# Kernel tuning notes

Measured on AMD Instinct MI355X. Metric: run time of the kernel, lower is better.

The kernel has to match this reference:

```python
import jax, jax.numpy as jnp
import numpy as np

NUM_JOINT_LIST = [8, 10, 12, 14, 16, 18, 20, 22, 24, 9, 13, 17]
NUM_GLOBAL_LIST = [1, 0, 1, 1, 0, 1, 1, 1, 0, 1, 1, 1]
M = len(NUM_JOINT_LIST)
B, T, JMAX = 16, 128, 24
H, HEADS, L, RANK = 256, 8, 4, 8
DH = H // HEADS
LAYERSCALE = 1e-4


def setup_inputs():
    key = jax.random.key(0)
    ks = jax.random.split(key, 40)
    m_idx = jax.random.randint(ks[0], (B,), 0, M)
    nj = jnp.array(NUM_JOINT_LIST)[m_idx]
    valid = jnp.arange(JMAX)[None, :] < nj[:, None]  # (B, J) real joints of each morphology
    jtype = jax.random.randint(ks[1], (B, JMAX), 0, 3)  # 0 slide, 1 hinge, 2 global
    has_g = (jnp.array(NUM_GLOBAL_LIST) > 0)[m_idx][:, None]
    jtype = jnp.where((jtype == 2) & ~has_g, 0, jtype)
    tile = lambda m: jnp.broadcast_to(m[:, None, :], (B, T, JMAX))
    slide_mask = tile((jtype == 0) & valid)
    hinge_mask = tile((jtype == 1) & valid)
    global_mask = tile((jtype == 2) & valid)
    act_mask = tile(valid)
    morph_mask = (valid[:, :, None] & valid[:, None, :]) | jnp.eye(JMAX, dtype=bool)[None]
    act = jax.random.normal(ks[2], (B, T, JMAX, 1), dtype=jnp.float32)
    s = 0.02
    inp = dict(act=act, slide_mask=slide_mask, hinge_mask=hinge_mask,
               global_mask=global_mask, act_mask=act_mask, morph_mask=morph_mask,
               m_idx=m_idx)
    inp['Ws'] = s * jax.random.normal(ks[3], (1, H)); inp['bs'] = jnp.zeros((H,))
    inp['Wh'] = s * jax.random.normal(ks[4], (1, H)); inp['bh'] = jnp.zeros((H,))
    inp['Wg'] = s * jax.random.normal(ks[5], (M, H))
    inp['Wact'] = s * jax.random.normal(ks[6], (1, H))
    pos = jax.random.normal(ks[7], (M, JMAX, H))
    pos_valid = jnp.arange(JMAX)[None, :, None] < jnp.array(NUM_JOINT_LIST)[:, None, None]
    inp['pos'] = pos * pos_valid  # rows beyond num_joint stay zero, as in the torch loop
    inp['ln1_s'] = jnp.ones((L, H)); inp['ln1_b'] = jnp.zeros((L, H))
    inp['Wqkv'] = s * jax.random.normal(ks[8], (L, H, 3 * H)); inp['bqkv'] = jnp.zeros((L, 3 * H))
    inp['loraA'] = s * jax.random.normal(ks[9], (L, M, H, RANK))
    inp['loraB'] = s * jax.random.normal(ks[10], (L, M, RANK, 3 * H))
    inp['Wo'] = s * jax.random.normal(ks[11], (L, H, H)); inp['bo'] = jnp.zeros((L, H))
    inp['ln2_s'] = jnp.ones((L, H)); inp['ln2_b'] = jnp.zeros((L, H))
    inp['W1'] = s * jax.random.normal(ks[12], (L, H, 4 * H)); inp['b1'] = jnp.zeros((L, 4 * H))
    inp['W2'] = s * jax.random.normal(ks[13], (L, 4 * H, H)); inp['b2'] = jnp.zeros((L, H))
    inp['g1'] = LAYERSCALE * jnp.ones((L, H)); inp['g2'] = LAYERSCALE * jnp.ones((L, H))
    inp['lnf_s'] = jnp.ones((H,)); inp['lnf_b'] = jnp.zeros((H,))
    return inp


def _ln(z, sc, bi):
    mu = z.mean(-1, keepdims=True)
    v = ((z - mu) ** 2).mean(-1, keepdims=True)
    return (z - mu) * jax.lax.rsqrt(v + 1e-5) * sc + bi


def reference(act, slide_mask, hinge_mask, global_mask, act_mask, morph_mask, m_idx,
              Ws, bs, Wh, bh, Wg, Wact, pos,
              ln1_s, ln1_b, Wqkv, bqkv, loraA, loraB, Wo, bo,
              ln2_s, ln2_b, W1, b1, W2, b2, g1, g2, lnf_s, lnf_b):
    has_g = (jnp.array(NUM_GLOBAL_LIST) > 0)[m_idx]  # (B,)
    a1 = act[..., :1]  # slide_dim = hinge_dim = num_global = 1
    emb = jnp.where(slide_mask[..., None], a1 @ Ws + bs, jnp.zeros((), act.dtype))
    emb = jnp.where(hinge_mask[..., None], a1 @ Wh + bh, emb)
    emb_g = a1 * Wg[m_idx][:, None, None, :]  # per-sample morphology-routed projection
    emb = jnp.where((global_mask & has_g[:, None, None])[..., None], emb_g, emb)
    y = emb + act_mask[..., None].astype(emb.dtype) * Wact[0]
    y = y + pos[m_idx][:, None]  # (B, T, J, H)
    Bv, Tv, J, _ = y.shape
    N = Bv * Tv
    x = y.reshape(N, J, H)
    amask = jnp.broadcast_to(morph_mask[:, None], (Bv, Tv, J, J)).reshape(N, J, J)
    t_idx = jnp.repeat(m_idx, Tv)  # (N,)
    neg = jnp.finfo(x.dtype).min
    scale = 1.0 / np.sqrt(DH)

    def block(x, lp):
        l1s, l1b, wqkv, bq, lA, lB, wo, bo_, l2s, l2b, w1, b1_, w2, b2_, gg1, gg2 = lp
        h = _ln(x, l1s, l1b)
        qkv = h @ wqkv + bq
        # per-task LoRA on qkv, gathered by morphology index
        qkv = qkv + jnp.einsum('njr,nrk->njk', jnp.einsum('njd,ndr->njr', h, lA[t_idx]), lB[t_idx])
        q, k, v = jnp.split(qkv, 3, axis=-1)
        q = q.reshape(N, J, HEADS, DH).transpose(0, 2, 1, 3)
        k = k.reshape(N, J, HEADS, DH).transpose(0, 2, 1, 3)
        v = v.reshape(N, J, HEADS, DH).transpose(0, 2, 1, 3)
        scores = jnp.einsum('nhid,nhjd->nhij', q, k) * scale
        scores = jnp.where(amask[:, None], scores, neg)
        attn = jax.nn.softmax(scores, axis=-1)
        o = jnp.einsum('nhij,nhjd->nhid', attn, v).transpose(0, 2, 1, 3).reshape(N, J, H)
        x = x + gg1 * (o @ wo + bo_)
        h2 = _ln(x, l2s, l2b)
        x = x + gg2 * (jax.nn.gelu(h2 @ w1 + b1_) @ w2 + b2_)
        return x, None

    x, _ = jax.lax.scan(block, x, (ln1_s, ln1_b, Wqkv, bqkv, loraA, loraB, Wo, bo,
                                   ln2_s, ln2_b, W1, b1, W2, b2, g1, g2))
    x = _ln(x, lnf_s, lnf_b)
    return x.reshape(Bv, Tv, J, H)
```

## Files before the change

### kernel.cpp

```cpp
#include <hip/hip_runtime.h>
#include <cstdint>
#include <cstddef>

#define B_     16
#define T_     128
#define J_     24
#define H_     256
#define HEADS_ 8
#define DH_    32
#define L_     4
#define RANK_  8
#define M_     12
#define NTOK   (B_*T_)
#define ROWS   (NTOK*J_)
#define HAS_G_MASK 3821

typedef __attribute__((ext_vector_type(8))) short short8;
typedef __attribute__((ext_vector_type(4))) float f32x4;

__constant__ int cNJ[M_] = {8, 10, 12, 14, 16, 18, 20, 22, 24, 9, 13, 17};

__device__ __forceinline__ float bf2f(unsigned short u) {
    union { unsigned int i; float f; } c; c.i = ((unsigned int)u) << 16; return c.f;
}
__device__ __forceinline__ unsigned short f2bf(float f) {
    union { float f; unsigned int i; } c; c.f = f;
    unsigned int x = c.i;
    return (unsigned short)((x + 0x7fffu + ((x >> 16) & 1u)) >> 16);
}
__device__ __forceinline__ float asf(unsigned int u) {
    union { unsigned int i; float f; } c; c.i = u; return c.f;
}
__device__ __forceinline__ void gload16(const void* g, void* l) {
    __builtin_amdgcn_global_load_lds((const __attribute__((address_space(1))) void*)g,
                                     (__attribute__((address_space(3))) void*)l, 16, 0, 0);
}

__global__ void zero_flag(int* f) { *f = 0; }

__global__ __launch_bounds__(256) void detect_kernel(
    const unsigned char* __restrict__ sl, const unsigned char* __restrict__ hi,
    const unsigned char* __restrict__ gl, const int* __restrict__ m_idx,
    int* __restrict__ flag) {
    int rj = blockIdx.x * 256 + threadIdx.x;
    if (rj >= ROWS) return;
    int b = rj / (T_ * J_);
    int j = rj % J_;
    int valid = (j < cNJ[m_idx[b]]) ? 1 : 0;
    int cnt = (sl[rj] != 0) + (hi[rj] != 0) + (gl[rj] != 0);
    if (cnt != valid) atomicOr(flag, 1);
}

__global__ void wconv_t(const float* __restrict__ W, unsigned short* __restrict__ WT,
                        int K, int Nc, int total) {
    int i = blockIdx.x * 256 + threadIdx.x;
    if (i >= total) return;
    int kn = K * Nc;
    int l = i / kn;
    int r = i - l * kn;
    int k = r / Nc;
    int n = r - k * Nc;
    WT[(size_t)l * kn + (size_t)n * K + k] = f2bf(W[i]);
}

__global__ __launch_bounds__(256) void embed_kernel(
    const float* __restrict__ act, const void* __restrict__ slide,
    const void* __restrict__ hinge, const void* __restrict__ glob,
    const int* __restrict__ m_idx, const int* __restrict__ flag,
    const float* __restrict__ Ws, const float* __restrict__ bs,
    const float* __restrict__ Wh, const float* __restrict__ bh,
    const float* __restrict__ Wg, const float* __restrict__ Wact,
    const float* __restrict__ pos, float* __restrict__ X) {
    int rj = (blockIdx.x << 2) + (threadIdx.x >> 6);
    int lane = threadIdx.x & 63;
    int b = rj / (T_ * J_);
    int j = rj % J_;
    int m = m_idx[b];
    bool valid = j < cNJ[m];
    bool s, hh, gl;
    if (*flag) {
        s  = ((const int*)slide)[rj] != 0;
        hh = ((const int*)hinge)[rj] != 0;
        gl = ((const int*)glob)[rj]  != 0;
    } else {
        s  = ((const unsigned char*)slide)[rj] != 0;
        hh = ((const unsigned char*)hinge)[rj] != 0;
        gl = ((const unsigned char*)glob)[rj]  != 0;
    }
    float a1 = act[rj];
    int h0 = lane << 2;
    float e0 = 0.f, e1 = 0.f, e2 = 0.f, e3 = 0.f;
    if (s) {
        float4 w = *(const float4*)(Ws + h0); float4 bb = *(const float4*)(bs + h0);
        e0 = a1 * w.x + bb.x; e1 = a1 * w.y + bb.y; e2 = a1 * w.z + bb.z; e3 = a1 * w.w + bb.w;
    } else if (hh) {
        float4 w = *(const float4*)(Wh + h0); float4 bb = *(const float4*)(bh + h0);
        e0 = a1 * w.x + bb.x; e1 = a1 * w.y + bb.y; e2 = a1 * w.z + bb.z; e3 = a1 * w.w + bb.w;
    } else if (gl && ((HAS_G_MASK >> m) & 1)) {
        float4 w = *(const float4*)(Wg + m * H_ + h0);
        e0 = a1 * w.x; e1 = a1 * w.y; e2 = a1 * w.z; e3 = a1 * w.w;
    }
    if (valid) {
        float4 wa = *(const float4*)(Wact + h0);
        e0 += wa.x; e1 += wa.y; e2 += wa.z; e3 += wa.w;
    }
    float4 pv = *(const float4*)(pos + (size_t)(m * J_ + j) * H_ + h0);
    float4 out; out.x = e0 + pv.x; out.y = e1 + pv.y; out.z = e2 + pv.z; out.w = e3 + pv.w;
    *(float4*)(X + ((size_t)rj << 8) + h0) = out;
}

template<bool LORA>
__global__ __launch_bounds__(256) void ln_kernel(
    const float* __restrict__ X, const float* __restrict__ sc, const float* __restrict__ bi,
    const float* __restrict__ lA, const int* __restrict__ m_idx,
    unsigned short* __restrict__ Hbf, float* __restrict__ Rbuf) {
    int row = (blockIdx.x << 2) + (threadIdx.x >> 6);
    int lane = threadIdx.x & 63;
    int h0 = lane << 2;
    float4 xv = *(const float4*)(X + ((size_t)row << 8) + h0);
    float s1 = xv.x + xv.y + xv.z + xv.w;
    float s2 = xv.x * xv.x + xv.y * xv.y + xv.z * xv.z + xv.w * xv.w;
    #pragma unroll
    for (int o = 32; o; o >>= 1) { s1 += __shfl_xor(s1, o); s2 += __shfl_xor(s2, o); }
    float mu = s1 * (1.f / H_);
    float var = s2 * (1.f / H_) - mu * mu;
    float rs = rsqrtf(var + 1e-5f);
    float4 scv = *(const float4*)(sc + h0);
    float4 biv = *(const float4*)(bi + h0);
    float hn0 = (xv.x - mu) * rs * scv.x + biv.x;
    float hn1 = (xv.y - mu) * rs * scv.y + biv.y;
    float hn2 = (xv.z - mu) * rs * scv.z + biv.z;
    float hn3 = (xv.w - mu) * rs * scv.w + biv.w;
    ushort4 o4; o4.x = f2bf(hn0); o4.y = f2bf(hn1); o4.z = f2bf(hn2); o4.w = f2bf(hn3);
    *(ushort4*)(Hbf + ((size_t)row << 8) + h0) = o4;
    if (LORA) {
        int t = m_idx[row / (J_ * T_)];
        const float* Ap = lA + (size_t)t * (H_ * RANK_) + h0 * RANK_;
        float4 av[8];
        #pragma unroll
        for (int c = 0; c < 8; ++c) av[c] = ((const float4*)Ap)[c];
        float hn[4] = {hn0, hn1, hn2, hn3};
        float p[RANK_];
        #pragma unroll
        for (int k = 0; k < RANK_; ++k) p[k] = 0.f;
        #pragma unroll
        for (int i = 0; i < 4; ++i)
            #pragma unroll
            for (int k = 0; k < RANK_; ++k) {
                int idx = i * RANK_ + k;
                float a = (idx & 3) == 0 ? av[idx >> 2].x : (idx & 3) == 1 ? av[idx >> 2].y
                        : (idx & 3) == 2 ? av[idx >> 2].z : av[idx >> 2].w;
                p[k] += hn[i] * a;
            }
        #pragma unroll
        for (int k = 0; k < RANK_; ++k)
            #pragma unroll
            for (int o = 32; o; o >>= 1) p[k] += __shfl_xor(p[k], o);
        if (lane == 0) {
            #pragma unroll
            for (int k = 0; k < RANK_; ++k) Rbuf[(size_t)row * RANK_ + k] = p[k];
        }
    }
}

__global__ __launch_bounds__(256) void lnf_kernel(
    float* __restrict__ X, const float* __restrict__ sc, const float* __restrict__ bi) {
    int row = (blockIdx.x << 2) + (threadIdx.x >> 6);
    int lane = threadIdx.x & 63;
    int h0 = lane << 2;
    float4 xv = *(const float4*)(X + ((size_t)row << 8) + h0);
    float s1 = xv.x + xv.y + xv.z + xv.w;
    float s2 = xv.x * xv.x + xv.y * xv.y + xv.z * xv.z + xv.w * xv.w;
    #pragma unroll
    for (int o = 32; o; o >>= 1) { s1 += __shfl_xor(s1, o); s2 += __shfl_xor(s2, o); }
    float mu = s1 * (1.f / H_);
    float var = s2 * (1.f / H_) - mu * mu;
    float rs = rsqrtf(var + 1e-5f);
    float4 scv = *(const float4*)(sc + h0);
    float4 biv = *(const float4*)(bi + h0);
    float4 out;
    out.x = (xv.x - mu) * rs * scv.x + biv.x;
    out.y = (xv.y - mu) * rs * scv.y + biv.y;
    out.z = (xv.z - mu) * rs * scv.z + biv.z;
    out.w = (xv.w - mu) * rs * scv.w + biv.w;
    *(float4*)(X + ((size_t)row << 8) + h0) = out;
}

template<int EPI>
__global__ __launch_bounds__(256) void gemm_k(
    const unsigned short* __restrict__ A, const unsigned short* __restrict__ BT,
    const float* __restrict__ bias,
    const float* __restrict__ aux1,
    const float* __restrict__ aux2,
    const int* __restrict__ m_idx,
    unsigned short* __restrict__ outB, float* __restrict__ outF,
    int K, int Nc) {
    __shared__ __align__(16) unsigned short As[128 * 64];
    __shared__ __align__(16) unsigned short Bs[128 * 64];
    int gx = gridDim.x;
    int nwg = gx * gridDim.y;
    int id = blockIdx.y * gx + blockIdx.x;
    int bx = blockIdx.x, by = blockIdx.y;
    if ((nwg & 7) == 0) {
        int q8 = nwg >> 3;
        int sid = (id & 7) * q8 + (id >> 3);
        bx = sid % gx; by = sid / gx;
    }
    int col0 = bx * 128;
    int row0 = by * 128;
    int tid = threadIdx.x;
    int wv = tid >> 6, lane = tid & 63;
    int wm = wv >> 1, wn = wv & 1;

    f32x4 acc[4][4];
    const f32x4 z = {0.f, 0.f, 0.f, 0.f};
    #pragma unroll
    for (int mi = 0; mi < 4; ++mi)
        #pragma unroll
        for (int ni = 0; ni < 4; ++ni) acc[mi][ni] = z;

    for (int k0 = 0; k0 < K; k0 += 64) {
        #pragma unroll
        for (int it = 0; it < 4; ++it) {
            int f = (tid << 4) + (it << 12);
            int r = f >> 7;
            int ce = (f & 127) >> 1;
            gload16(A  + (size_t)(row0 + r) * K + k0 + ce, (char*)As + f);
            gload16(BT + (size_t)(col0 + r) * K + k0 + ce, (char*)Bs + f);
        }
        __syncthreads();
        #pragma unroll
        for (int kk = 0; kk < 64; kk += 32) {
            short8 af[4], bfr[4];
            int ko = kk + ((lane >> 4) << 3);
            #pragma unroll
            for (int q = 0; q < 4; ++q) {
                af[q]  = *(const short8*)(As + ((wm * 64 + q * 16 + (lane & 15)) << 6) + ko);
                bfr[q] = *(const short8*)(Bs + ((wn * 64 + q * 16 + (lane & 15)) << 6) + ko);
            }
            #pragma unroll
            for (int mi = 0; mi < 4; ++mi)
                #pragma unroll
                for (int ni = 0; ni < 4; ++ni)
                    acc[mi][ni] = __builtin_amdgcn_mfma_f32_16x16x32_bf16(af[mi], bfr[ni], acc[mi][ni], 0, 0, 0);
        }
        __syncthreads();
    }

    int rbase = row0 + wm * 64 + ((lane >> 4) << 2);
    int cbase = col0 + wn * 64 + (lane & 15);

    if (EPI == 0) {
        int t = m_idx[row0 / (J_ * T_)];
        const float* lB = aux2 + (size_t)t * (RANK_ * 3 * H_);
        float lbv[4][RANK_];
        #pragma unroll
        for (int ni = 0; ni < 4; ++ni)
            #pragma unroll
            for (int kq = 0; kq < RANK_; ++kq)
                lbv[ni][kq] = lB[kq * (3 * H_) + cbase + ni * 16];
        #pragma unroll
        for (int mi = 0; mi < 4; ++mi) {
            #pragma unroll
            for (int r = 0; r < 4; ++r) {
                int row = rbase + mi * 16 + r;
                const float* Rr = aux1 + (size_t)row * RANK_;
                float rv[RANK_];
                #pragma unroll
                for (int kq = 0; kq < RANK_; ++kq) rv[kq] = Rr[kq];
                #pragma unroll
                for (int ni = 0; ni < 4; ++ni) {
                    int col = cbase + ni * 16;
                    float val = acc[mi][ni][r] + bias[col];
                    #pragma unroll
                    for (int kq = 0; kq < RANK_; ++kq) val += rv[kq] * lbv[ni][kq];
                    outB[(size_t)row * (3 * H_) + col] = f2bf(val);
                }
            }
        }
    } else if (EPI == 1) {
        #pragma unroll
        for (int mi = 0; mi < 4; ++mi)
            #pragma unroll
            for (int r = 0; r < 4; ++r) {
                int row = rbase + mi * 16 + r;
                #pragma unroll
                for (int ni = 0; ni < 4; ++ni) {
                    int col = cbase + ni * 16;
                    float u = acc[mi][ni][r] + bias[col];
                    float zz = 0.7978845608028654f * (u + 0.044715f * u * u * u);
                    float tt = __expf(-2.f * fabsf(zz));
                    float th = (1.f - tt) / (1.f + tt);
                    th = zz < 0.f ? -th : th;
                    outB[(size_t)row * Nc + col] = f2bf(0.5f * u * (1.f + th));
                }
            }
    } else {
        #pragma unroll
        for (int mi = 0; mi < 4; ++mi)
            #pragma unroll
            for (int r = 0; r < 4; ++r) {
                int row = rbase + mi * 16 + r;
                #pragma unroll
                for (int ni = 0; ni < 4; ++ni) {
                    int col = cbase + ni * 16;
                    float u = acc[mi][ni][r] + bias[col];
                    outF[(size_t)row * H_ + col] += aux1[col] * u;
                }
            }
    }
}

__global__ __launch_bounds__(256) void attn_kernel(
    const unsigned short* __restrict__ QKV, const int* __restrict__ m_idx,
    unsigned short* __restrict__ O) {
    __shared__ unsigned int q2s[4][24][18];
    __shared__ unsigned int k2s[4][16][26];
    __shared__ unsigned int v2s[4][24][18];
    __shared__ float       scs[4][24][27];
    int w = threadIdx.x >> 6, lane = threadIdx.x & 63;
    int n = blockIdx.x >> 1;
    int hd = ((blockIdx.x & 1) << 2) + w;
    int nj = cNJ[m_idx[n >> 7]];
    unsigned int (*q2)[18] = q2s[w];
    unsigned int (*k2)[26] = k2s[w];
    unsigned int (*v2)[18] = v2s[w];
    float (*sc)[27] = scs[w];

    const unsigned short* base = QKV + (size_t)n * (J_ * 768) + hd * DH_;

    #pragma unroll
    for (int it = 0; it < 3; ++it) {
        int r = it * 64 + lane;
        int j = r >> 3, d0 = (r & 7) << 2, d2 = d0 >> 1;
        ushort4 x = *(const ushort4*)(base + (size_t)j * 768 + d0);
        q2[j][d2]     = (unsigned int)x.x | ((unsigned int)x.y << 16);
        q2[j][d2 + 1] = (unsigned int)x.z | ((unsigned int)x.w << 16);
    }
    #pragma unroll
    for (int it = 0; it < 3; ++it) {
        int r = it * 64 + lane;
        int j = r >> 3, d0 = (r & 7) << 2, d2 = d0 >> 1;
        ushort4 x = *(const ushort4*)(base + (size_t)j * 768 + 256 + d0);
        k2[d2][j]     = (unsigned int)x.x | ((unsigned int)x.y << 16);
        k2[d2 + 1][j] = (unsigned int)x.z | ((unsigned int)x.w << 16);
    }
    #pragma unroll
    for (int it = 0; it < 3; ++it) {
        int r = it * 64 + lane;
        int j = r >> 3, d0 = (r & 7) << 2, d2 = d0 >> 1;
        ushort4 x = *(const ushort4*)(base + (size_t)j * 768 + 512 + d0);
        v2[j][d2]     = (unsigned int)x.x | ((unsigned int)x.y << 16);
        v2[j][d2 + 1] = (unsigned int)x.z | ((unsigned int)x.w << 16);
    }

    int i = lane >> 1, half = lane & 1;
    if (lane < 48) {
        float qf[32];
        #pragma unroll
        for (int d2 = 0; d2 < 16; ++d2) {
            unsigned int x = q2[i][d2];
            qf[2 * d2]     = asf(x << 16);
            qf[2 * d2 + 1] = asf(x & 0xffff0000u);
        }
        int jb = half * 12;
        float s[12];
        #pragma unroll
        for (int jj = 0; jj < 12; ++jj) {
            int j = jb + jj;
            float acc = 0.f;
            #pragma unroll
            for (int d2 = 0; d2 < 16; ++d2) {
                unsigned int x = k2[d2][j];
                acc += qf[2 * d2] * asf(x << 16);
                acc += qf[2 * d2 + 1] * asf(x & 0xffff0000u);
            }
            bool ok = (i < nj && j < nj) || (i == j);
            s[jj] = ok ? acc * 0.17677669529663687f : -1e30f;
        }
        float mx = s[0];
        #pragma unroll
        for (int jj = 1; jj < 12; ++jj) mx = fmaxf(mx, s[jj]);
        mx = fmaxf(mx, __shfl_xor(mx, 1));
        float sm = 0.f;
        #pragma unroll
        for (int jj = 0; jj < 12; ++jj) { float e = __expf(s[jj] - mx); s[jj] = e; sm += e; }
        sm += __shfl_xor(sm, 1);
        float inv = 1.f / sm;
        #pragma unroll
        for (int jj = 0; jj < 12; ++jj) sc[i][jb + jj] = s[jj] * inv;
    }

    #pragma unroll
    for (int it = 0; it < 6; ++it) {
        int i2 = it * 4 + (lane >> 4), d2 = lane & 15;
        float olo = 0.f, ohi = 0.f;
        #pragma unroll
        for (int j = 0; j < J_; ++j) {
            float p = sc[i2][j];
            unsigned int x = v2[j][d2];
            olo += p * asf(x << 16);
            ohi += p * asf(x & 0xffff0000u);
        }
        unsigned int o = (unsigned int)f2bf(olo) | ((unsigned int)f2bf(ohi) << 16);
        *(unsigned int*)(O + (size_t)(n * J_ + i2) * H_ + hd * DH_ + 2 * d2) = o;
    }
}

extern "C" void kernel_launch(void* const* d_in, const int* in_sizes, int n_in,
                              void* d_out, int out_size, void* d_ws, size_t ws_size,
                              hipStream_t stream) {
    (void)in_sizes; (void)n_in; (void)out_size; (void)ws_size;
    const float* act   = (const float*)d_in[0];
    const void*  slide = d_in[1];
    const void*  hinge = d_in[2];
    const void*  glob  = d_in[3];
    const int* m_idx  = (const int*)d_in[6];
    const float* Ws   = (const float*)d_in[7];
    const float* bs   = (const float*)d_in[8];
    const float* Wh   = (const float*)d_in[9];
    const float* bh   = (const float*)d_in[10];
    const float* Wg   = (const float*)d_in[11];
    const float* Wact = (const float*)d_in[12];
    const float* pos  = (const float*)d_in[13];
    const float* ln1s = (const float*)d_in[14];
    const float* ln1b = (const float*)d_in[15];
    const float* Wqkv = (const float*)d_in[16];
    const float* bqkv = (const float*)d_in[17];
    const float* loraA= (const float*)d_in[18];
    const float* loraB= (const float*)d_in[19];
    const float* Wo   = (const float*)d_in[20];
    const float* bo   = (const float*)d_in[21];
    const float* ln2s = (const float*)d_in[22];
    const float* ln2b = (const float*)d_in[23];
    const float* W1   = (const float*)d_in[24];
    const float* b1   = (const float*)d_in[25];
    const float* W2   = (const float*)d_in[26];
    const float* b2   = (const float*)d_in[27];
    const float* g1   = (const float*)d_in[28];
    const float* g2   = (const float*)d_in[29];
    const float* lnfs = (const float*)d_in[30];
    const float* lnfb = (const float*)d_in[31];

    float* X = (float*)d_out;

    size_t off = 0;
    char* ws = (char*)d_ws;
    auto nxt = [&](size_t bytes) -> char* {
        char* p = ws + off; off += (bytes + 255) & ~(size_t)255; return p;
    };
    int*            dflag = (int*)nxt(256);
    unsigned short* Hbf   = (unsigned short*)nxt((size_t)ROWS * H_ * 2);
    unsigned short* QKVG  = (unsigned short*)nxt((size_t)ROWS * 1024 * 2);
    float*          Rbuf  = (float*)nxt((size_t)ROWS * RANK_ * 4);
    unsigned short* WqkvT = (unsigned short*)nxt((size_t)L_ * H_ * 768 * 2);
    unsigned short* WoT   = (unsigned short*)nxt((size_t)L_ * H_ * H_ * 2);
    unsigned short* W1T   = (unsigned short*)nxt((size_t)L_ * H_ * 1024 * 2);
    unsigned short* W2T   = (unsigned short*)nxt((size_t)L_ * 1024 * H_ * 2);
    unsigned short* Obf   = Hbf;

    zero_flag<<<1, 1, 0, stream>>>(dflag);
    detect_kernel<<<(ROWS + 255) / 256, 256, 0, stream>>>(
        (const unsigned char*)slide, (const unsigned char*)hinge,
        (const unsigned char*)glob, m_idx, dflag);

    wconv_t<<<(L_ * H_ * 768 + 255) / 256, 256, 0, stream>>>(Wqkv, WqkvT, H_, 768, L_ * H_ * 768);
    wconv_t<<<(L_ * H_ * H_  + 255) / 256, 256, 0, stream>>>(Wo,   WoT,   H_, H_,  L_ * H_ * H_);
    wconv_t<<<(L_ * H_ * 1024+ 255) / 256, 256, 0, stream>>>(W1,   W1T,   H_, 1024,L_ * H_ * 1024);
    wconv_t<<<(L_ * 1024* H_ + 255) / 256, 256, 0, stream>>>(W2,   W2T,   1024, H_,L_ * 1024 * H_);

    embed_kernel<<<ROWS / 4, 256, 0, stream>>>(act, slide, hinge, glob, m_idx, dflag,
                                               Ws, bs, Wh, bh, Wg, Wact, pos, X);

    for (int l = 0; l < L_; ++l) {
        ln_kernel<true><<<ROWS / 4, 256, 0, stream>>>(X, ln1s + l * H_, ln1b + l * H_,
                                                      loraA + (size_t)l * M_ * H_ * RANK_, m_idx, Hbf, Rbuf);
        gemm_k<0><<<dim3(6, 384), 256, 0, stream>>>(Hbf, WqkvT + (size_t)l * H_ * 768,
                                                    bqkv + l * 768, Rbuf,
                                                    loraB + (size_t)l * M_ * RANK_ * 768, m_idx,
                                                    QKVG, nullptr, H_, 768);
        attn_kernel<<<NTOK * 2, 256, 0, stream>>>(QKVG, m_idx, Obf);
        gemm_k<2><<<dim3(2, 384), 256, 0, stream>>>(Obf, WoT + (size_t)l * H_ * H_,
                                                    bo + l * H_, g1 + l * H_, nullptr, nullptr,
                                                    nullptr, X, H_, H_);
        ln_kernel<false><<<ROWS / 4, 256, 0, stream>>>(X, ln2s + l * H_, ln2b + l * H_,
                                                       nullptr, nullptr, Hbf, nullptr);
        gemm_k<1><<<dim3(8, 384), 256, 0, stream>>>(Hbf, W1T + (size_t)l * H_ * 1024,
                                                    b1 + l * 1024, nullptr, nullptr, nullptr,
                                                    QKVG, nullptr, H_, 1024);
        gemm_k<2><<<dim3(2, 384), 256, 0, stream>>>(QKVG, W2T + (size_t)l * 1024 * H_,
                                                    b2 + l * H_, g2 + l * H_, nullptr, nullptr,
                                                    nullptr, X, 1024, H_);
    }

    lnf_kernel<<<ROWS / 4, 256, 0, stream>>>(X, lnfs, lnfb);
}
```

Before: 1.445 ms.

## Fold LoRA-B into per-morphology augmented QKV weights and pack bf16 epilogue stores

The LoRA low-rank projection is written as extra bf16 columns of the LN output (K widened to 320), and Wqkv is concatenated with each morphology's loraB into a per-task weight matrix, so the QKV GEMM absorbs the LoRA-B product instead of running it in the epilogue. The QKV and GELU epilogues now swap values between lane pairs and pack them with v_cvt_pk_bf16_f32 into 32-bit stores. GELU uses the sigmoid form of the tanh approximation, and the weight transpose kernel now writes coalesced instead of reading coalesced. The cost is a larger per-morphology weight buffer and 25% more K in the QKV GEMM, mostly zero padding, plus LoRA intermediates rounded to bf16.

```diff
diff --git a/kernel.cpp b/kernel.cpp
--- a/kernel.cpp
+++ b/kernel.cpp
@@ -13,6 +13,7 @@
 #define M_     12
 #define NTOK   (B_*T_)
 #define ROWS   (NTOK*J_)
+#define KQ     320
 #define HAS_G_MASK 3821
 
 typedef __attribute__((ext_vector_type(8))) short short8;
@@ -30,6 +31,11 @@
 }
 __device__ __forceinline__ float asf(unsigned int u) {
     union { unsigned int i; float f; } c; c.i = u; return c.f;
+}
+__device__ __forceinline__ unsigned int cvtpk(float lo, float hi) {
+    unsigned int r;
+    asm("v_cvt_pk_bf16_f32 %0, %1, %2" : "=v"(r) : "v"(lo), "v"(hi));
+    return r;
 }
 __device__ __forceinline__ void gload16(const void* g, void* l) {
     __builtin_amdgcn_global_load_lds((const __attribute__((address_space(1))) void*)g,
@@ -58,9 +64,24 @@
     int kn = K * Nc;
     int l = i / kn;
     int r = i - l * kn;
-    int k = r / Nc;
-    int n = r - k * Nc;
-    WT[(size_t)l * kn + (size_t)n * K + k] = f2bf(W[i]);
+    int n = r / K;
+    int k = r - n * K;
+    WT[i] = f2bf(W[(size_t)l * kn + (size_t)k * Nc + n]);
+}
+
+__global__ void wconv_qkv(const float* __restrict__ Wqkv, const float* __restrict__ loraB,
+                          unsigned short* __restrict__ OT) {
+    int i = blockIdx.x * 256 + threadIdx.x;
+    const int total = L_ * M_ * 768 * KQ;
+    if (i >= total) return;
+    int k = i % KQ;
+    int n = (i / KQ) % 768;
+    int m = (i / (KQ * 768)) % M_;
+    int l = i / (KQ * 768 * M_);
+    float v = 0.f;
+    if (k < 256)      v = Wqkv[((size_t)l * 256 + k) * 768 + n];
+    else if (k < 264) v = loraB[(((size_t)l * M_ + m) * RANK_ + (k - 256)) * 768 + n];
+    OT[i] = f2bf(v);
 }
 
 __global__ __launch_bounds__(256) void embed_kernel(
@@ -113,7 +134,7 @@
 __global__ __launch_bounds__(256) void ln_kernel(
     const float* __restrict__ X, const float* __restrict__ sc, const float* __restrict__ bi,
     const float* __restrict__ lA, const int* __restrict__ m_idx,
-    unsigned short* __restrict__ Hbf, float* __restrict__ Rbuf) {
+    unsigned short* __restrict__ Hbf, int ldh) {
     int row = (blockIdx.x << 2) + (threadIdx.x >> 6);
     int lane = threadIdx.x & 63;
     int h0 = lane << 2;
@@ -132,7 +153,7 @@
     float hn2 = (xv.z - mu) * rs * scv.z + biv.z;
     float hn3 = (xv.w - mu) * rs * scv.w + biv.w;
     ushort4 o4; o4.x = f2bf(hn0); o4.y = f2bf(hn1); o4.z = f2bf(hn2); o4.w = f2bf(hn3);
-    *(ushort4*)(Hbf + ((size_t)row << 8) + h0) = o4;
+    *(ushort4*)(Hbf + (size_t)row * ldh + h0) = o4;
     if (LORA) {
         int t = m_idx[row / (J_ * T_)];
         const float* Ap = lA + (size_t)t * (H_ * RANK_) + h0 * RANK_;
@@ -156,10 +177,15 @@
         for (int k = 0; k < RANK_; ++k)
             #pragma unroll
             for (int o = 32; o; o >>= 1) p[k] += __shfl_xor(p[k], o);
-        if (lane == 0) {
-            #pragma unroll
-            for (int k = 0; k < RANK_; ++k) Rbuf[(size_t)row * RANK_ + k] = p[k];
-        }
+        unsigned int w0 = (unsigned int)f2bf(p[0]) | ((unsigned int)f2bf(p[1]) << 16);
+        unsigned int w1 = (unsigned int)f2bf(p[2]) | ((unsigned int)f2bf(p[3]) << 16);
+        unsigned int w2 = (unsigned int)f2bf(p[4]) | ((unsigned int)f2bf(p[5]) << 16);
+        unsigned int w3 = (unsigned int)f2bf(p[6]) | ((unsigned int)f2bf(p[7]) << 16);
+        unsigned int tv = 0;
+        if (lane == 0) tv = w0; else if (lane == 1) tv = w1;
+        else if (lane == 2) tv = w2; else if (lane == 3) tv = w3;
+        if (lane < 32)
+            *((unsigned int*)(Hbf + (size_t)row * ldh + 256) + lane) = tv;
     }
 }
 
@@ -191,7 +217,6 @@
     const unsigned short* __restrict__ A, const unsigned short* __restrict__ BT,
     const float* __restrict__ bias,
     const float* __restrict__ aux1,
-    const float* __restrict__ aux2,
     const int* __restrict__ m_idx,
     unsigned short* __restrict__ outB, float* __restrict__ outF,
     int K, int Nc) {
@@ -212,6 +237,8 @@
     int wv = tid >> 6, lane = tid & 63;
     int wm = wv >> 1, wn = wv & 1;
 
+    if (EPI == 0) BT += (size_t)m_idx[row0 / (J_ * T_)] * (768 * KQ);
+
     f32x4 acc[4][4];
     const f32x4 z = {0.f, 0.f, 0.f, 0.f};
     #pragma unroll
@@ -250,51 +277,40 @@
     int rbase = row0 + wm * 64 + ((lane >> 4) << 2);
     int cbase = col0 + wn * 64 + (lane & 15);
 
-    if (EPI == 0) {
-        int t = m_idx[row0 / (J_ * T_)];
-        const float* lB = aux2 + (size_t)t * (RANK_ * 3 * H_);
-        float lbv[4][RANK_];
-        #pragma unroll
-        for (int ni = 0; ni < 4; ++ni)
-            #pragma unroll
-            for (int kq = 0; kq < RANK_; ++kq)
-                lbv[ni][kq] = lB[kq * (3 * H_) + cbase + ni * 16];
-        #pragma unroll
-        for (int mi = 0; mi < 4; ++mi) {
-            #pragma unroll
-            for (int r = 0; r < 4; ++r) {
-                int row = rbase + mi * 16 + r;
-                const float* Rr = aux1 + (size_t)row * RANK_;
-                float rv[RANK_];
+    if (EPI == 0 || EPI == 1) {
+        const int ld = (EPI == 0) ? 768 : Nc;
+        bool oddl = (lane & 1);
+        int colp = cbase - (oddl ? 1 : 0);
+        #pragma unroll
+        for (int ni = 0; ni < 4; ++ni) {
+            float bv = bias[cbase + ni * 16];
+            #pragma unroll
+            for (int mi = 0; mi < 4; ++mi) {
+                float v[4], y[4];
                 #pragma unroll
-                for (int kq = 0; kq < RANK_; ++kq) rv[kq] = Rr[kq];
+                for (int r = 0; r < 4; ++r) {
+                    float u = acc[mi][ni][r] + bv;
+                    if (EPI == 1) {
+                        float t = u * u;
+                        float p = fmaf(t, 0.044715f, 1.0f) * u;
+                        float e = __expf(-1.5957691216057308f * p);
+                        u = u / (1.f + e);
+                    }
+                    v[r] = u;
+                }
                 #pragma unroll
-                for (int ni = 0; ni < 4; ++ni) {
-                    int col = cbase + ni * 16;
-                    float val = acc[mi][ni][r] + bias[col];
-                    #pragma unroll
-                    for (int kq = 0; kq < RANK_; ++kq) val += rv[kq] * lbv[ni][kq];
-                    outB[(size_t)row * (3 * H_) + col] = f2bf(val);
-                }
+                for (int r = 0; r < 4; ++r) y[r] = __shfl_xor(v[r], 1);
+                float f0 = oddl ? y[2] : v[0];
+                float s0 = oddl ? v[2] : y[0];
+                float f1 = oddl ? y[3] : v[1];
+                float s1 = oddl ? v[3] : y[1];
+                unsigned int p0 = cvtpk(f0, s0);
+                unsigned int p1 = cvtpk(f1, s1);
+                int rr = rbase + mi * 16 + (oddl ? 2 : 0);
+                *(unsigned int*)(outB + (size_t)rr * ld + colp + ni * 16) = p0;
+                *(unsigned int*)(outB + (size_t)(rr + 1) * ld + colp + ni * 16) = p1;
             }
         }
-    } else if (EPI == 1) {
-        #pragma unroll
-        for (int mi = 0; mi < 4; ++mi)
-            #pragma unroll
-            for (int r = 0; r < 4; ++r) {
-                int row = rbase + mi * 16 + r;
-                #pragma unroll
-                for (int ni = 0; ni < 4; ++ni) {
-                    int col = cbase + ni * 16;
-                    float u = acc[mi][ni][r] + bias[col];
-                    float zz = 0.7978845608028654f * (u + 0.044715f * u * u * u);
-                    float tt = __expf(-2.f * fabsf(zz));
-                    float th = (1.f - tt) / (1.f + tt);
-                    th = zz < 0.f ? -th : th;
-                    outB[(size_t)row * Nc + col] = f2bf(0.5f * u * (1.f + th));
-                }
-            }
     } else {
         #pragma unroll
         for (int mi = 0; mi < 4; ++mi)
@@ -449,47 +465,45 @@
     auto nxt = [&](size_t bytes) -> char* {
         char* p = ws + off; off += (bytes + 255) & ~(size_t)255; return p;
     };
-    int*            dflag = (int*)nxt(256);
-    unsigned short* Hbf   = (unsigned short*)nxt((size_t)ROWS * H_ * 2);
-    unsigned short* QKVG  = (unsigned short*)nxt((size_t)ROWS * 1024 * 2);
-    float*          Rbuf  = (float*)nxt((size_t)ROWS * RANK_ * 4);
-    unsigned short* WqkvT = (unsigned short*)nxt((size_t)L_ * H_ * 768 * 2);
-    unsigned short* WoT   = (unsigned short*)nxt((size_t)L_ * H_ * H_ * 2);
-    unsigned short* W1T   = (unsigned short*)nxt((size_t)L_ * H_ * 1024 * 2);
-    unsigned short* W2T   = (unsigned short*)nxt((size_t)L_ * 1024 * H_ * 2);
-    unsigned short* Obf   = Hbf;
+    int*            dflag  = (int*)nxt(256);
+    unsigned short* Hbf    = (unsigned short*)nxt((size_t)ROWS * KQ * 2);
+    unsigned short* QKVG   = (unsigned short*)nxt((size_t)ROWS * 1024 * 2);
+    unsigned short* WqkvTp = (unsigned short*)nxt((size_t)L_ * M_ * 768 * KQ * 2);
+    unsigned short* WoT    = (unsigned short*)nxt((size_t)L_ * H_ * H_ * 2);
+    unsigned short* W1T    = (unsigned short*)nxt((size_t)L_ * H_ * 1024 * 2);
+    unsigned short* W2T    = (unsigned short*)nxt((size_t)L_ * 1024 * H_ * 2);
+    unsigned short* Obf    = Hbf;
 
     zero_flag<<<1, 1, 0, stream>>>(dflag);
     detect_kernel<<<(ROWS + 255) / 256, 256, 0, stream>>>(
         (const unsigned char*)slide, (const unsigned char*)hinge,
         (const unsigned char*)glob, m_idx, dflag);
 
-    wconv_t<<<(L_ * H_ * 768 + 255) / 256, 256, 0, stream>>>(Wqkv, WqkvT, H_, 768, L_ * H_ * 768);
-    wconv_t<<<(L_ * H_ * H_  + 255) / 256, 256, 0, stream>>>(Wo,   WoT,   H_, H_,  L_ * H_ * H_);
-    wconv_t<<<(L_ * H_ * 1024+ 255) / 256, 256, 0, stream>>>(W1,   W1T,   H_, 1024,L_ * H_ * 1024);
-    wconv_t<<<(L_ * 1024* H_ + 255) / 256, 256, 0, stream>>>(W2,   W2T,   1024, H_,L_ * 1024 * H_);
+    wconv_qkv<<<(L_ * M_ * 768 * KQ + 255) / 256, 256, 0, stream>>>(Wqkv, loraB, WqkvTp);
+    wconv_t<<<(L_ * H_ * H_   + 255) / 256, 256, 0, stream>>>(Wo, WoT, H_, H_,   L_ * H_ * H_);
+    wconv_t<<<(L_ * H_ * 1024 + 255) / 256, 256, 0, stream>>>(W1, W1T, H_, 1024, L_ * H_ * 1024);
+    wconv_t<<<(L_ * 1024 * H_ + 255) / 256, 256, 0, stream>>>(W2, W2T, 1024, H_, L_ * 1024 * H_);
 
     embed_kernel<<<ROWS / 4, 256, 0, stream>>>(act, slide, hinge, glob, m_idx, dflag,
                                                Ws, bs, Wh, bh, Wg, Wact, pos, X);
 
     for (int l = 0; l < L_; ++l) {
         ln_kernel<true><<<ROWS / 4, 256, 0, stream>>>(X, ln1s + l * H_, ln1b + l * H_,
-                                                      loraA + (size_t)l * M_ * H_ * RANK_, m_idx, Hbf, Rbuf);
-        gemm_k<0><<<dim3(6, 384), 256, 0, stream>>>(Hbf, WqkvT + (size_t)l * H_ * 768,
-                                                    bqkv + l * 768, Rbuf,
-                                                    loraB + (size_t)l * M_ * RANK_ * 768, m_idx,
-                                                    QKVG, nullptr, H_, 768);
+                                                      loraA + (size_t)l * M_ * H_ * RANK_, m_idx, Hbf, KQ);
+        gemm_k<0><<<dim3(6, 384), 256, 0, stream>>>(Hbf, WqkvTp + (size_t)l * M_ * 768 * KQ,
+                                                    bqkv + l * 768, nullptr, m_idx,
+                                                    QKVG, nullptr, KQ, 768);
         attn_kernel<<<NTOK * 2, 256, 0, stream>>>(QKVG, m_idx, Obf);
         gemm_k<2><<<dim3(2, 384), 256, 0, stream>>>(Obf, WoT + (size_t)l * H_ * H_,
-                                                    bo + l * H_, g1 + l * H_, nullptr, nullptr,
+                                                    bo + l * H_, g1 + l * H_, nullptr,
                                                     nullptr, X, H_, H_);
         ln_kernel<false><<<ROWS / 4, 256, 0, stream>>>(X, ln2s + l * H_, ln2b + l * H_,
-                                                       nullptr, nullptr, Hbf, nullptr);
+                                                       nullptr, nullptr, Hbf, H_);
         gemm_k<1><<<dim3(8, 384), 256, 0, stream>>>(Hbf, W1T + (size_t)l * H_ * 1024,
-                                                    b1 + l * 1024, nullptr, nullptr, nullptr,
+                                                    b1 + l * 1024, nullptr, nullptr,
                                                     QKVG, nullptr, H_, 1024);
         gemm_k<2><<<dim3(2, 384), 256, 0, stream>>>(QKVG, W2T + (size_t)l * 1024 * H_,
-                                                    b2 + l * H_, g2 + l * H_, nullptr, nullptr,
+                                                    b2 + l * H_, g2 + l * H_, nullptr,
                                                     nullptr, X, 1024, H_);
     }
 
```

Result: no change. 1.449 ms (+0.3%).
